# Optimization experiments

Measured on AMD Instinct MI355X. Metric: run time of the kernel, lower is better.

Reference implementation:

```python
import jax, jax.numpy as jnp
import numpy as np

N_NODES = 50000
N_EDGES = 600000
DIM = 128
N_LAYERS = 2


def setup_inputs() -> dict:
    key = jax.random.key(0)
    ks = jax.random.split(key, 4)
    x = jax.random.normal(ks[0], (N_NODES, DIM), dtype=jnp.float32)
    edge_index = jax.random.randint(ks[1], (2, N_EDGES), 0, N_NODES, dtype=jnp.int32)
    # xavier_normal-ish scale for transform (fan_in=fan_out=DIM) and gate
    Wt = jax.random.normal(ks[2], (N_LAYERS, DIM, DIM), dtype=jnp.float32) * (1.414 * (2.0 / (2 * DIM)) ** 0.5)
    Wg = jax.random.normal(ks[3], (N_LAYERS, DIM), dtype=jnp.float32) * (1.414 * (2.0 / (DIM + 1)) ** 0.5)
    bt = jnp.zeros((N_LAYERS, DIM), dtype=jnp.float32)
    bg = jnp.zeros((N_LAYERS,), dtype=jnp.float32)
    return {"x": x, "edge_index": edge_index, "Wt": Wt, "bt": bt, "Wg": Wg, "bg": bg}


def _fa_layer(h, row, col, Wt_l, bt_l, Wg_l, bg_l):
    # h: [N, D]. transform
    h = h @ Wt_l.T + bt_l
    n = h.shape[0]
    ones = jnp.ones(row.shape, dtype=h.dtype)
    deg = jnp.clip(jax.ops.segment_sum(ones, row, num_segments=n), 1.0)
    dinv = deg ** -0.5  # [N]
    # per-edge gate on source node features
    g = jnp.tanh(h[row] @ Wg_l + bg_l)  # [E]
    norm = g * dinv[row] * dinv[col]    # [E]
    msg = norm[:, None] * h[row]        # [E, D]
    out = jax.ops.segment_sum(msg, col, num_segments=n)
    return out + h


def reference(x, edge_index, Wt, bt, Wg, bg):
    row, col = edge_index[0], edge_index[1]
    h = x
    for l in range(N_LAYERS):
        h = _fa_layer(h, row, col, Wt[l], bt[l], Wg[l], bg[l])
        h = jax.nn.relu(h)  # dropout p=0 / eval -> identity
    return h
```

## Files before the change

### kernel.cpp

```cpp
#include <hip/hip_runtime.h>
#include <cstdint>
#include <cstddef>

#define DIM 128
#define BM 128
#define NB1 128
#define RBITS 14
#define RSIZE (1 << RBITS)
#define NB2 32

typedef __attribute__((ext_vector_type(8))) short bf16x8;
typedef __attribute__((ext_vector_type(16))) float f32x16;

__device__ inline unsigned short f2b(float x) {
    unsigned int u = __float_as_uint(x);
    unsigned int r = (u + 0x7fffu + ((u >> 16) & 1u)) >> 16;
    return (unsigned short)r;
}
__device__ inline float blo(unsigned int u) { return __uint_as_float(u << 16); }
__device__ inline float bhi(unsigned int u) { return __uint_as_float(u & 0xffff0000u); }

__global__ __launch_bounds__(256) void bucket_hist_kernel(
    const int* __restrict__ col, int* __restrict__ counts,
    int E, int chunk, int nbuk, int bshift)
{
    extern __shared__ int hs[];
    for (int i = threadIdx.x; i < nbuk; i += 256) hs[i] = 0;
    __syncthreads();
    int e0 = blockIdx.x * chunk;
    int e1 = min(E, e0 + chunk);
    for (int e = e0 + threadIdx.x; e < e1; e += 256)
        atomicAdd(&hs[col[e] >> bshift], 1);
    __syncthreads();
    int* out = counts + (size_t)blockIdx.x * nbuk;
    for (int i = threadIdx.x; i < nbuk; i += 256) out[i] = hs[i];
}

__global__ __launch_bounds__(256) void col_scan_kernel(
    int* __restrict__ counts, int* __restrict__ tot, int nbuk)
{
    int w = threadIdx.x >> 6;
    int lane = threadIdx.x & 63;
    int t = blockIdx.x * 4 + w;
    if (t >= nbuk) return;
    int c0 = counts[(size_t)(lane * 2) * nbuk + t];
    int c1 = counts[(size_t)(lane * 2 + 1) * nbuk + t];
    int s = c0 + c1;
    int x = s;
#pragma unroll
    for (int d = 1; d < 64; d <<= 1) {
        int y = __shfl_up(x, (unsigned)d, 64);
        if (lane >= d) x += y;
    }
    int excl = x - s;
    counts[(size_t)(lane * 2) * nbuk + t] = excl;
    counts[(size_t)(lane * 2 + 1) * nbuk + t] = excl + c0;
    if (lane == 63) tot[t] = x;
}

__global__ __launch_bounds__(1024) void bstart_scan_kernel(
    const int* __restrict__ tot, int* __restrict__ bstart, int nbuk, int E)
{
    __shared__ int buf[1024];
    int t = threadIdx.x;
    int v = (t < nbuk) ? tot[t] : 0;
    buf[t] = v;
    __syncthreads();
    for (int s = 1; s < 1024; s <<= 1) {
        int x = (t >= s) ? buf[t - s] : 0;
        __syncthreads();
        buf[t] += x;
        __syncthreads();
    }
    if (t < nbuk) bstart[t] = buf[t] - v;
    if (t == 0) bstart[nbuk] = E;
}

__global__ __launch_bounds__(256) void bucket_scatter_kernel(
    const int* __restrict__ row, const int* __restrict__ col,
    const int* __restrict__ bases, const int* __restrict__ bstart,
    unsigned int* __restrict__ tmp,
    int E, int chunk, int nbuk, int bshift)
{
    extern __shared__ int cur[];
    const int* mybase = bases + (size_t)blockIdx.x * nbuk;
    for (int i = threadIdx.x; i < nbuk; i += 256) cur[i] = mybase[i] + bstart[i];
    __syncthreads();
    int e0 = blockIdx.x * chunk;
    int e1 = min(E, e0 + chunk);
    int rsh = 32 - bshift;
    unsigned int smask = (1u << bshift) - 1u;
    for (int e = e0 + threadIdx.x; e < e1; e += 256) {
        int c = col[e];
        int pos = atomicAdd(&cur[c >> bshift], 1);
        tmp[pos] = (((unsigned int)c & smask) << rsh) | (unsigned int)row[e];
    }
}

__global__ __launch_bounds__(256) void bucket_group_kernel(
    const unsigned int* __restrict__ tmp, const int* __restrict__ bstart,
    int* __restrict__ off, int* __restrict__ csr, int n, int E, int bshift)
{
    __shared__ int subh[4096];
    const int b = blockIdx.x;
    const int tid = threadIdx.x;
    const int subb = 1 << bshift;
    const int rsh = 32 - bshift;
    const unsigned int rmask = (1u << rsh) - 1u;
    int beg = bstart[b], end = bstart[b + 1];

    for (int i = tid; i < subb; i += 256) subh[i] = 0;
    __syncthreads();
    for (int i = beg + tid; i < end; i += 256)
        atomicAdd(&subh[tmp[i] >> rsh], 1);
    __syncthreads();
    if (subb <= 64) {
        if (tid < 64) {
            int v = (tid < subb) ? subh[tid] : 0;
            int x = v;
            for (int d = 1; d < 64; d <<= 1) {
                int y = __shfl_up(x, (unsigned)d, 64);
                if (tid >= d) x += y;
            }
            if (tid < subb) subh[tid] = x - v;
        }
    } else {
        if (tid == 0) {
            int run = 0;
            for (int i = 0; i < subb; ++i) { int c = subh[i]; subh[i] = run; run += c; }
        }
    }
    __syncthreads();
    int c0 = b << bshift;
    for (int i = tid; i < subb; i += 256) {
        int c = c0 + i;
        if (c < n) off[c] = beg + subh[i];
    }
    if (b == gridDim.x - 1 && tid == 0) off[n] = E;
    __syncthreads();
    for (int i = beg + tid; i < end; i += 256) {
        unsigned int v = tmp[i];
        int rank = atomicAdd(&subh[v >> rsh], 1);
        csr[beg + rank] = (int)(v & rmask);
    }
}

__global__ __launch_bounds__(256) void deg_hist_kernel(
    const int* __restrict__ row, int* __restrict__ gcounts, int E)
{
    __shared__ int hs[RSIZE];
    int r = blockIdx.x / NB2, bi = blockIdx.x % NB2;
    for (int i = threadIdx.x; i < RSIZE; i += 256) hs[i] = 0;
    __syncthreads();
    int chunk = (E + NB2 - 1) / NB2;
    int e0 = bi * chunk, e1 = min(E, e0 + chunk);
    for (int e = e0 + threadIdx.x; e < e1; e += 256) {
        int rv = row[e];
        if ((rv >> RBITS) == r) atomicAdd(&hs[rv & (RSIZE - 1)], 1);
    }
    __syncthreads();
    int* out = gcounts + (size_t)blockIdx.x * RSIZE;
    for (int i = threadIdx.x; i < RSIZE; i += 256) out[i] = hs[i];
}

__global__ __launch_bounds__(256) void dinv_kernel(
    const int* __restrict__ gcounts, float* __restrict__ dinv, int n)
{
    int i = blockIdx.x * 256 + threadIdx.x;
    if (i >= n) return;
    int r = i >> RBITS, bl = i & (RSIZE - 1);
    int s = 0;
    for (int bi = 0; bi < NB2; ++bi)
        s += gcounts[(size_t)(r * NB2 + bi) * RSIZE + bl];
    dinv[i] = rsqrtf((float)max(s, 1));
}

__global__ __launch_bounds__(256) void transform_kernel(
    const float* __restrict__ hin, const float* __restrict__ Wt,
    const float* __restrict__ bt, const float* __restrict__ Wg,
    const float* __restrict__ bg, const float* __restrict__ dinv,
    unsigned short* __restrict__ h1b, float* __restrict__ aout, int n)
{
    __shared__ __align__(16) unsigned short h_s[BM * DIM];
    __shared__ __align__(16) unsigned short w_s[DIM * DIM];
    __shared__ float p_s[BM];

    const int tid = threadIdx.x;
    const int node0 = blockIdx.x * BM;
    const int lane = tid & 63;
    const int wv = tid >> 6;

#pragma unroll
    for (int it = 0; it < 16; ++it) {
        int g = it * 256 + tid;
        int r = g >> 5;
        int c4 = g & 31;
        int src = node0 + r;
        if (src >= n) src = n - 1;
        float4 hv = *(const float4*)(hin + (size_t)src * DIM + c4 * 4);
        float4 wvv = *(const float4*)(Wt + (size_t)r * DIM + c4 * 4);
        int chunk = (c4 >> 1) ^ (r & 15);
        int base = r * DIM + chunk * 8 + (c4 & 1) * 4;
        h_s[base + 0] = f2b(hv.x); h_s[base + 1] = f2b(hv.y);
        h_s[base + 2] = f2b(hv.z); h_s[base + 3] = f2b(hv.w);
        w_s[base + 0] = f2b(wvv.x); w_s[base + 1] = f2b(wvv.y);
        w_s[base + 2] = f2b(wvv.z); w_s[base + 3] = f2b(wvv.w);
    }
    __syncthreads();

    f32x16 acc[4] = {};
    const int l31 = lane & 31;
    const int asel = lane >> 5;
    const int swz = l31 & 15;
    const unsigned short* ha = h_s + (wv * 32 + l31) * DIM;
#pragma unroll
    for (int ks = 0; ks < 8; ++ks) {
        int ch = ((ks * 2 + asel) ^ swz) * 8;
        bf16x8 av = *(const bf16x8*)(ha + ch);
#pragma unroll
        for (int cf = 0; cf < 4; ++cf) {
            bf16x8 bv = *(const bf16x8*)(w_s + (cf * 32 + l31) * DIM + ch);
            acc[cf] = __builtin_amdgcn_mfma_f32_32x32x16_bf16(av, bv, acc[cf], 0, 0, 0);
        }
    }
    __syncthreads();

    float btc[4], wgc[4];
#pragma unroll
    for (int cf = 0; cf < 4; ++cf) {
        btc[cf] = bt[cf * 32 + l31];
        wgc[cf] = Wg[cf * 32 + l31];
    }
    float p[16];
#pragma unroll
    for (int q = 0; q < 16; ++q) p[q] = 0.0f;
#pragma unroll
    for (int cf = 0; cf < 4; ++cf) {
#pragma unroll
        for (int q = 0; q < 16; ++q) {
            float v = acc[cf][q] + btc[cf];
            p[q] = fmaf(v, wgc[cf], p[q]);
            int row = (q & 3) + 8 * (q >> 2) + 4 * asel;
            h_s[(wv * 32 + row) * DIM + cf * 32 + l31] = f2b(v);
        }
    }
#pragma unroll
    for (int m = 1; m < 32; m <<= 1) {
#pragma unroll
        for (int q = 0; q < 16; ++q) p[q] += __shfl_xor(p[q], m, 64);
    }
    if (l31 == 0) {
#pragma unroll
        for (int q = 0; q < 16; ++q) {
            int row = (q & 3) + 8 * (q >> 2) + 4 * asel;
            p_s[wv * 32 + row] = p[q];
        }
    }
    __syncthreads();

#pragma unroll
    for (int it = 0; it < 8; ++it) {
        int g = it * 256 + tid;
        int r = g >> 4;
        int c = g & 15;
        int4 v = *(const int4*)(h_s + r * DIM + c * 8);
        int dst = node0 + r;
        if (dst < n) *(int4*)(h1b + (size_t)dst * DIM + c * 8) = v;
    }

    if (tid < BM) {
        int node = node0 + tid;
        if (node < n) aout[node] = tanhf(p_s[tid] + bg[0]) * dinv[node];
    }
}

__global__ __launch_bounds__(256) void agg_kernel(
    const int* __restrict__ off, const int* __restrict__ csr_row,
    const float* __restrict__ a, const float* __restrict__ dinv,
    const unsigned short* __restrict__ h1b, float* __restrict__ out, int n)
{
    int node = blockIdx.x * 4 + (threadIdx.x >> 6);
    if (node >= n) return;
    int lane = threadIdx.x & 63;
    int beg = off[node], end = off[node + 1];
    const unsigned int* hb = (const unsigned int*)h1b;
    float s0x = 0.f, s0y = 0.f, s1x = 0.f, s1y = 0.f;
    float s2x = 0.f, s2y = 0.f, s3x = 0.f, s3y = 0.f;
    int s = beg;
    for (; s + 4 <= end; s += 4) {
        int r0 = csr_row[s], r1 = csr_row[s + 1], r2 = csr_row[s + 2], r3 = csr_row[s + 3];
        float a0 = a[r0], a1 = a[r1], a2 = a[r2], a3 = a[r3];
        unsigned int u0 = hb[(size_t)r0 * 64 + lane];
        unsigned int u1 = hb[(size_t)r1 * 64 + lane];
        unsigned int u2 = hb[(size_t)r2 * 64 + lane];
        unsigned int u3 = hb[(size_t)r3 * 64 + lane];
        s0x = fmaf(a0, blo(u0), s0x); s0y = fmaf(a0, bhi(u0), s0y);
        s1x = fmaf(a1, blo(u1), s1x); s1y = fmaf(a1, bhi(u1), s1y);
        s2x = fmaf(a2, blo(u2), s2x); s2y = fmaf(a2, bhi(u2), s2y);
        s3x = fmaf(a3, blo(u3), s3x); s3y = fmaf(a3, bhi(u3), s3y);
    }
    for (; s < end; ++s) {
        int r0 = csr_row[s];
        float a0 = a[r0];
        unsigned int u0 = hb[(size_t)r0 * 64 + lane];
        s0x = fmaf(a0, blo(u0), s0x); s0y = fmaf(a0, bhi(u0), s0y);
    }
    float dv = dinv[node];
    unsigned int ur = hb[(size_t)node * 64 + lane];
    float2 o;
    o.x = fmaxf(fmaf(dv, s0x + s1x + s2x + s3x, blo(ur)), 0.0f);
    o.y = fmaxf(fmaf(dv, s0y + s1y + s2y + s3y, bhi(ur)), 0.0f);
    ((float2*)out)[(size_t)node * 64 + lane] = o;
}

extern "C" void kernel_launch(void* const* d_in, const int* in_sizes, int n_in,
                              void* d_out, int out_size, void* d_ws, size_t ws_size,
                              hipStream_t stream) {
    const float* x    = (const float*)d_in[0];
    const int*   edge = (const int*)d_in[1];
    const float* Wt   = (const float*)d_in[2];
    const float* bt   = (const float*)d_in[3];
    const float* Wg   = (const float*)d_in[4];
    const float* bg   = (const float*)d_in[5];
    float* out = (float*)d_out;

    const int n = in_sizes[0] / DIM;
    const int E = in_sizes[1] / 2;
    const int* row = edge;
    const int* col = edge + E;

    int bshift = 6;
    while (((n + (1 << bshift) - 1) >> bshift) > 1024) ++bshift;
    const int nbuk = (n + (1 << bshift) - 1) >> bshift;
    const int nr = (n + RSIZE - 1) >> RBITS;

    char* base = (char*)d_ws;
    size_t o = 0;
    auto carve = [&](size_t bytes) -> void* {
        void* p = base + o;
        o += (bytes + 255) & ~(size_t)255;
        return p;
    };
    unsigned short* h1b  = (unsigned short*)carve((size_t)n * DIM * 2);
    float* dinv          = (float*)carve((size_t)n * 4);
    float* a             = (float*)carve((size_t)n * 4);
    int*   off           = (int*)carve((size_t)(n + 1) * 4);
    int*   csr           = (int*)carve((size_t)E * 4);
    unsigned int* tmp    = (unsigned int*)carve((size_t)E * 4);
    int*   counts        = (int*)carve((size_t)NB1 * nbuk * 4);
    int*   bstart        = (int*)carve((size_t)(nbuk + 1) * 4);
    int*   tot           = (int*)carve((size_t)nbuk * 4);
    int*   gcounts       = (int*)carve((size_t)nr * NB2 * RSIZE * 4);

    const int chunk1 = (E + NB1 - 1) / NB1;
    const size_t ldsb = (size_t)nbuk * 4;

    deg_hist_kernel<<<nr * NB2, 256, 0, stream>>>(row, gcounts, E);
    dinv_kernel<<<(n + 255) / 256, 256, 0, stream>>>(gcounts, dinv, n);

    bucket_hist_kernel<<<NB1, 256, ldsb, stream>>>(col, counts, E, chunk1, nbuk, bshift);
    col_scan_kernel<<<(nbuk + 3) / 4, 256, 0, stream>>>(counts, tot, nbuk);
    bstart_scan_kernel<<<1, 1024, 0, stream>>>(tot, bstart, nbuk, E);
    bucket_scatter_kernel<<<NB1, 256, ldsb, stream>>>(row, col, counts, bstart, tmp, E, chunk1, nbuk, bshift);
    bucket_group_kernel<<<nbuk, 256, 0, stream>>>(tmp, bstart, off, csr, n, E, bshift);

    const int gt = (n + BM - 1) / BM;
    for (int l = 0; l < 2; ++l) {
        const float* hin = (l == 0) ? x : out;
        const float* Wtl = Wt + (size_t)l * DIM * DIM;
        const float* btl = bt + (size_t)l * DIM;
        const float* Wgl = Wg + (size_t)l * DIM;
        const float* bgl = bg + l;

        transform_kernel<<<gt, 256, 0, stream>>>(
            hin, Wtl, btl, Wgl, bgl, dinv, h1b, a, n);
        agg_kernel<<<(n + 3) / 4, 256, 0, stream>>>(off, csr, a, dinv, h1b, out, n);
    }
}
```

Measured before the change: 158.4 us.

## Merge CSR-build kernels and pass bf16 intermediate between layers

```diff
diff --git a/kernel.cpp b/kernel.cpp
--- a/kernel.cpp
+++ b/kernel.cpp
@@ -20,77 +20,121 @@
 __device__ inline float blo(unsigned int u) { return __uint_as_float(u << 16); }
 __device__ inline float bhi(unsigned int u) { return __uint_as_float(u & 0xffff0000u); }
 
-__global__ __launch_bounds__(256) void bucket_hist_kernel(
-    const int* __restrict__ col, int* __restrict__ counts,
-    int E, int chunk, int nbuk, int bshift)
-{
-    extern __shared__ int hs[];
-    for (int i = threadIdx.x; i < nbuk; i += 256) hs[i] = 0;
-    __syncthreads();
-    int e0 = blockIdx.x * chunk;
-    int e1 = min(E, e0 + chunk);
-    for (int e = e0 + threadIdx.x; e < e1; e += 256)
-        atomicAdd(&hs[col[e] >> bshift], 1);
-    __syncthreads();
-    int* out = counts + (size_t)blockIdx.x * nbuk;
-    for (int i = threadIdx.x; i < nbuk; i += 256) out[i] = hs[i];
-}
-
-__global__ __launch_bounds__(256) void col_scan_kernel(
-    int* __restrict__ counts, int* __restrict__ tot, int nbuk)
-{
-    int w = threadIdx.x >> 6;
-    int lane = threadIdx.x & 63;
-    int t = blockIdx.x * 4 + w;
-    if (t >= nbuk) return;
-    int c0 = counts[(size_t)(lane * 2) * nbuk + t];
-    int c1 = counts[(size_t)(lane * 2 + 1) * nbuk + t];
-    int s = c0 + c1;
-    int x = s;
-#pragma unroll
-    for (int d = 1; d < 64; d <<= 1) {
-        int y = __shfl_up(x, (unsigned)d, 64);
-        if (lane >= d) x += y;
-    }
-    int excl = x - s;
-    counts[(size_t)(lane * 2) * nbuk + t] = excl;
-    counts[(size_t)(lane * 2 + 1) * nbuk + t] = excl + c0;
-    if (lane == 63) tot[t] = x;
-}
-
-__global__ __launch_bounds__(1024) void bstart_scan_kernel(
-    const int* __restrict__ tot, int* __restrict__ bstart, int nbuk, int E)
-{
-    __shared__ int buf[1024];
+__global__ __launch_bounds__(256) void hists_kernel(
+    const int* __restrict__ row, const int* __restrict__ col,
+    int* __restrict__ gcounts, int* __restrict__ counts,
+    int E, int ndeg, int nbuk, int bshift)
+{
+    __shared__ int hs[RSIZE];
+    int b = blockIdx.x;
+    if (b < ndeg) {
+        int r = b / NB2, bi = b % NB2;
+        for (int i = threadIdx.x; i < RSIZE; i += 256) hs[i] = 0;
+        __syncthreads();
+        int chunk = (E + NB2 - 1) / NB2;
+        int e0 = bi * chunk, e1 = min(E, e0 + chunk);
+        for (int e = e0 + threadIdx.x; e < e1; e += 256) {
+            int rv = row[e];
+            if ((rv >> RBITS) == r) atomicAdd(&hs[rv & (RSIZE - 1)], 1);
+        }
+        __syncthreads();
+        int* outp = gcounts + (size_t)b * RSIZE;
+        for (int i = threadIdx.x; i < RSIZE; i += 256) outp[i] = hs[i];
+    } else {
+        int hb = b - ndeg;
+        for (int i = threadIdx.x; i < nbuk; i += 256) hs[i] = 0;
+        __syncthreads();
+        int chunk = (E + NB1 - 1) / NB1;
+        int e0 = hb * chunk, e1 = min(E, e0 + chunk);
+        for (int e = e0 + threadIdx.x; e < e1; e += 256)
+            atomicAdd(&hs[col[e] >> bshift], 1);
+        __syncthreads();
+        int* outp = counts + (size_t)hb * nbuk;
+        for (int i = threadIdx.x; i < nbuk; i += 256) outp[i] = hs[i];
+    }
+}
+
+__global__ __launch_bounds__(256) void scan_dinv_kernel(
+    int* __restrict__ counts, int* __restrict__ tot,
+    const int* __restrict__ gcounts, float* __restrict__ dinv,
+    int nbuk, int n, int nscan)
+{
+    int b = blockIdx.x;
+    if (b < nscan) {
+        int w = threadIdx.x >> 6;
+        int lane = threadIdx.x & 63;
+        int t = b * 4 + w;
+        if (t >= nbuk) return;
+        int c0 = counts[(size_t)(lane * 2) * nbuk + t];
+        int c1 = counts[(size_t)(lane * 2 + 1) * nbuk + t];
+        int s = c0 + c1;
+        int x = s;
+#pragma unroll
+        for (int d = 1; d < 64; d <<= 1) {
+            int y = __shfl_up(x, (unsigned)d, 64);
+            if (lane >= d) x += y;
+        }
+        int excl = x - s;
+        counts[(size_t)(lane * 2) * nbuk + t] = excl;
+        counts[(size_t)(lane * 2 + 1) * nbuk + t] = excl + c0;
+        if (lane == 63) tot[t] = x;
+    } else {
+        int i = (b - nscan) * 256 + threadIdx.x;
+        if (i >= n) return;
+        int r = i >> RBITS, bl = i & (RSIZE - 1);
+        int s = 0;
+        for (int bi = 0; bi < NB2; ++bi)
+            s += gcounts[(size_t)(r * NB2 + bi) * RSIZE + bl];
+        dinv[i] = rsqrtf((float)max(s, 1));
+    }
+}
+
+__global__ __launch_bounds__(256) void scatter_kernel(
+    const int* __restrict__ row, const int* __restrict__ col,
+    const int* __restrict__ bases, const int* __restrict__ tot,
+    unsigned int* __restrict__ tmp, int* __restrict__ bstart,
+    int E, int nbuk, int bshift)
+{
+    __shared__ int scanbuf[256];
+    __shared__ int bst[1024];
+    __shared__ int cur[1024];
     int t = threadIdx.x;
-    int v = (t < nbuk) ? tot[t] : 0;
-    buf[t] = v;
-    __syncthreads();
-    for (int s = 1; s < 1024; s <<= 1) {
-        int x = (t >= s) ? buf[t - s] : 0;
-        __syncthreads();
-        buf[t] += x;
-        __syncthreads();
-    }
-    if (t < nbuk) bstart[t] = buf[t] - v;
-    if (t == 0) bstart[nbuk] = E;
-}
-
-__global__ __launch_bounds__(256) void bucket_scatter_kernel(
-    const int* __restrict__ row, const int* __restrict__ col,
-    const int* __restrict__ bases, const int* __restrict__ bstart,
-    unsigned int* __restrict__ tmp,
-    int E, int chunk, int nbuk, int bshift)
-{
-    extern __shared__ int cur[];
+    int v[4];
+    int s = 0;
+#pragma unroll
+    for (int k = 0; k < 4; ++k) {
+        int idx = t * 4 + k;
+        v[k] = (idx < nbuk) ? tot[idx] : 0;
+        s += v[k];
+    }
+    scanbuf[t] = s;
+    __syncthreads();
+    for (int d = 1; d < 256; d <<= 1) {
+        int y = (t >= d) ? scanbuf[t - d] : 0;
+        __syncthreads();
+        scanbuf[t] += y;
+        __syncthreads();
+    }
+    int run = scanbuf[t] - s;
+#pragma unroll
+    for (int k = 0; k < 4; ++k) {
+        int idx = t * 4 + k;
+        if (idx < nbuk) bst[idx] = run;
+        run += v[k];
+    }
+    __syncthreads();
     const int* mybase = bases + (size_t)blockIdx.x * nbuk;
-    for (int i = threadIdx.x; i < nbuk; i += 256) cur[i] = mybase[i] + bstart[i];
-    __syncthreads();
-    int e0 = blockIdx.x * chunk;
-    int e1 = min(E, e0 + chunk);
+    for (int i = t; i < nbuk; i += 256) cur[i] = bst[i] + mybase[i];
+    if (blockIdx.x == 0) {
+        for (int i = t; i < nbuk; i += 256) bstart[i] = bst[i];
+        if (t == 0) bstart[nbuk] = E;
+    }
+    __syncthreads();
+    int chunk = (E + NB1 - 1) / NB1;
+    int e0 = blockIdx.x * chunk, e1 = min(E, e0 + chunk);
     int rsh = 32 - bshift;
     unsigned int smask = (1u << bshift) - 1u;
-    for (int e = e0 + threadIdx.x; e < e1; e += 256) {
+    for (int e = e0 + t; e < e1; e += 256) {
         int c = col[e];
         int pos = atomicAdd(&cur[c >> bshift], 1);
         tmp[pos] = (((unsigned int)c & smask) << rsh) | (unsigned int)row[e];
@@ -145,38 +189,9 @@
     }
 }
 
-__global__ __launch_bounds__(256) void deg_hist_kernel(
-    const int* __restrict__ row, int* __restrict__ gcounts, int E)
-{
-    __shared__ int hs[RSIZE];
-    int r = blockIdx.x / NB2, bi = blockIdx.x % NB2;
-    for (int i = threadIdx.x; i < RSIZE; i += 256) hs[i] = 0;
-    __syncthreads();
-    int chunk = (E + NB2 - 1) / NB2;
-    int e0 = bi * chunk, e1 = min(E, e0 + chunk);
-    for (int e = e0 + threadIdx.x; e < e1; e += 256) {
-        int rv = row[e];
-        if ((rv >> RBITS) == r) atomicAdd(&hs[rv & (RSIZE - 1)], 1);
-    }
-    __syncthreads();
-    int* out = gcounts + (size_t)blockIdx.x * RSIZE;
-    for (int i = threadIdx.x; i < RSIZE; i += 256) out[i] = hs[i];
-}
-
-__global__ __launch_bounds__(256) void dinv_kernel(
-    const int* __restrict__ gcounts, float* __restrict__ dinv, int n)
-{
-    int i = blockIdx.x * 256 + threadIdx.x;
-    if (i >= n) return;
-    int r = i >> RBITS, bl = i & (RSIZE - 1);
-    int s = 0;
-    for (int bi = 0; bi < NB2; ++bi)
-        s += gcounts[(size_t)(r * NB2 + bi) * RSIZE + bl];
-    dinv[i] = rsqrtf((float)max(s, 1));
-}
-
+template <bool BF16IN>
 __global__ __launch_bounds__(256) void transform_kernel(
-    const float* __restrict__ hin, const float* __restrict__ Wt,
+    const void* __restrict__ hin_v, const float* __restrict__ Wt,
     const float* __restrict__ bt, const float* __restrict__ Wg,
     const float* __restrict__ bg, const float* __restrict__ dinv,
     unsigned short* __restrict__ h1b, float* __restrict__ aout, int n)
@@ -197,12 +212,20 @@
         int c4 = g & 31;
         int src = node0 + r;
         if (src >= n) src = n - 1;
-        float4 hv = *(const float4*)(hin + (size_t)src * DIM + c4 * 4);
-        float4 wvv = *(const float4*)(Wt + (size_t)r * DIM + c4 * 4);
         int chunk = (c4 >> 1) ^ (r & 15);
         int base = r * DIM + chunk * 8 + (c4 & 1) * 4;
-        h_s[base + 0] = f2b(hv.x); h_s[base + 1] = f2b(hv.y);
-        h_s[base + 2] = f2b(hv.z); h_s[base + 3] = f2b(hv.w);
+        if constexpr (BF16IN) {
+            const unsigned short* hin = (const unsigned short*)hin_v;
+            ushort4 hv = *(const ushort4*)(hin + (size_t)src * DIM + c4 * 4);
+            h_s[base + 0] = hv.x; h_s[base + 1] = hv.y;
+            h_s[base + 2] = hv.z; h_s[base + 3] = hv.w;
+        } else {
+            const float* hin = (const float*)hin_v;
+            float4 hv = *(const float4*)(hin + (size_t)src * DIM + c4 * 4);
+            h_s[base + 0] = f2b(hv.x); h_s[base + 1] = f2b(hv.y);
+            h_s[base + 2] = f2b(hv.z); h_s[base + 3] = f2b(hv.w);
+        }
+        float4 wvv = *(const float4*)(Wt + (size_t)r * DIM + c4 * 4);
         w_s[base + 0] = f2b(wvv.x); w_s[base + 1] = f2b(wvv.y);
         w_s[base + 2] = f2b(wvv.z); w_s[base + 3] = f2b(wvv.w);
     }
@@ -274,10 +297,11 @@
     }
 }
 
+template <bool BF16OUT>
 __global__ __launch_bounds__(256) void agg_kernel(
     const int* __restrict__ off, const int* __restrict__ csr_row,
     const float* __restrict__ a, const float* __restrict__ dinv,
-    const unsigned short* __restrict__ h1b, float* __restrict__ out, int n)
+    const unsigned short* __restrict__ h1b, void* __restrict__ out_v, int n)
 {
     int node = blockIdx.x * 4 + (threadIdx.x >> 6);
     if (node >= n) return;
@@ -307,10 +331,14 @@
     }
     float dv = dinv[node];
     unsigned int ur = hb[(size_t)node * 64 + lane];
-    float2 o;
-    o.x = fmaxf(fmaf(dv, s0x + s1x + s2x + s3x, blo(ur)), 0.0f);
-    o.y = fmaxf(fmaf(dv, s0y + s1y + s2y + s3y, bhi(ur)), 0.0f);
-    ((float2*)out)[(size_t)node * 64 + lane] = o;
+    float ox = fmaxf(fmaf(dv, s0x + s1x + s2x + s3x, blo(ur)), 0.0f);
+    float oy = fmaxf(fmaf(dv, s0y + s1y + s2y + s3y, bhi(ur)), 0.0f);
+    if constexpr (BF16OUT) {
+        unsigned int pk = (unsigned int)f2b(ox) | ((unsigned int)f2b(oy) << 16);
+        ((unsigned int*)out_v)[(size_t)node * 64 + lane] = pk;
+    } else {
+        ((float2*)out_v)[(size_t)node * 64 + lane] = make_float2(ox, oy);
+    }
 }
 
 extern "C" void kernel_launch(void* const* d_in, const int* in_sizes, int n_in,
@@ -333,6 +361,7 @@
     while (((n + (1 << bshift) - 1) >> bshift) > 1024) ++bshift;
     const int nbuk = (n + (1 << bshift) - 1) >> bshift;
     const int nr = (n + RSIZE - 1) >> RBITS;
+    const int ndeg = nr * NB2;
 
     char* base = (char*)d_ws;
     size_t o = 0;
@@ -342,6 +371,7 @@
         return p;
     };
     unsigned short* h1b  = (unsigned short*)carve((size_t)n * DIM * 2);
+    unsigned short* hbuf = (unsigned short*)carve((size_t)n * DIM * 2);
     float* dinv          = (float*)carve((size_t)n * 4);
     float* a             = (float*)carve((size_t)n * 4);
     int*   off           = (int*)carve((size_t)(n + 1) * 4);
@@ -350,30 +380,26 @@
     int*   counts        = (int*)carve((size_t)NB1 * nbuk * 4);
     int*   bstart        = (int*)carve((size_t)(nbuk + 1) * 4);
     int*   tot           = (int*)carve((size_t)nbuk * 4);
-    int*   gcounts       = (int*)carve((size_t)nr * NB2 * RSIZE * 4);
-
-    const int chunk1 = (E + NB1 - 1) / NB1;
-    const size_t ldsb = (size_t)nbuk * 4;
-
-    deg_hist_kernel<<<nr * NB2, 256, 0, stream>>>(row, gcounts, E);
-    dinv_kernel<<<(n + 255) / 256, 256, 0, stream>>>(gcounts, dinv, n);
-
-    bucket_hist_kernel<<<NB1, 256, ldsb, stream>>>(col, counts, E, chunk1, nbuk, bshift);
-    col_scan_kernel<<<(nbuk + 3) / 4, 256, 0, stream>>>(counts, tot, nbuk);
-    bstart_scan_kernel<<<1, 1024, 0, stream>>>(tot, bstart, nbuk, E);
-    bucket_scatter_kernel<<<NB1, 256, ldsb, stream>>>(row, col, counts, bstart, tmp, E, chunk1, nbuk, bshift);
+    int*   gcounts       = (int*)carve((size_t)ndeg * RSIZE * 4);
+
+    hists_kernel<<<ndeg + NB1, 256, 0, stream>>>(row, col, gcounts, counts,
+                                                 E, ndeg, nbuk, bshift);
+    const int nscan = (nbuk + 3) / 4;
+    const int ndinv = (n + 255) / 256;
+    scan_dinv_kernel<<<nscan + ndinv, 256, 0, stream>>>(counts, tot, gcounts, dinv,
+                                                        nbuk, n, nscan);
+    scatter_kernel<<<NB1, 256, 0, stream>>>(row, col, counts, tot, tmp, bstart,
+                                            E, nbuk, bshift);
     bucket_group_kernel<<<nbuk, 256, 0, stream>>>(tmp, bstart, off, csr, n, E, bshift);
 
     const int gt = (n + BM - 1) / BM;
-    for (int l = 0; l < 2; ++l) {
-        const float* hin = (l == 0) ? x : out;
-        const float* Wtl = Wt + (size_t)l * DIM * DIM;
-        const float* btl = bt + (size_t)l * DIM;
-        const float* Wgl = Wg + (size_t)l * DIM;
-        const float* bgl = bg + l;
-
-        transform_kernel<<<gt, 256, 0, stream>>>(
-            hin, Wtl, btl, Wgl, bgl, dinv, h1b, a, n);
-        agg_kernel<<<(n + 3) / 4, 256, 0, stream>>>(off, csr, a, dinv, h1b, out, n);
-    }
-}
+    const int ga = (n + 3) / 4;
+
+    transform_kernel<false><<<gt, 256, 0, stream>>>(
+        x, Wt, bt, Wg, bg, dinv, h1b, a, n);
+    agg_kernel<true><<<ga, 256, 0, stream>>>(off, csr, a, dinv, h1b, hbuf, n);
+
+    transform_kernel<true><<<gt, 256, 0, stream>>>(
+        hbuf, Wt + DIM * DIM, bt + DIM, Wg + DIM, bg + 1, dinv, h1b, a, n);
+    agg_kernel<false><<<ga, 256, 0, stream>>>(off, csr, a, dinv, h1b, out, n);
+}
```

Measured after the change: 149.6 us. 5.5% less time.
